# Kernel tuning notes

Measured on AMD Instinct MI355X. Metric: run time of the kernel, lower is better.

Reference implementation:

```python
import jax, jax.numpy as jnp
import numpy as np

D_IN = 2048
D_OUT = 2048
N_HEADS = 32
N_KV = 8
HEAD_DIM = D_OUT // N_HEADS  # 64
CTX = 2048
ROPE_BASE = 10000.0


def _rope_tables(head_dim, ctx, base):
    inv_freq = 1.0 / base ** (np.arange(0, head_dim, 2, dtype=np.float32) / head_dim)
    pos = np.arange(ctx, dtype=np.float32)
    ang = pos[:, None] * inv_freq[None, :]          # [ctx, hd/2]
    ang = np.concatenate([ang, ang], axis=1)         # [ctx, hd]
    return jnp.asarray(np.cos(ang)), jnp.asarray(np.sin(ang))


def _apply_rope(x, cos, sin):
    # x: [b, h, n, hd]; cos/sin: [n, hd]
    half = x.shape[-1] // 2
    x1, x2 = x[..., :half], x[..., half:]
    rotated = jnp.concatenate([-x2, x1], axis=-1)
    return x * cos + rotated * sin


def setup_inputs() -> dict:
    key = jax.random.key(0)
    ks = jax.random.split(key, 5)
    b, n = 1, 2048
    x = jax.random.normal(ks[0], (b, n, D_IN), dtype=jnp.float32)
    s = 0.02
    Wq = jax.random.normal(ks[1], (D_IN, D_OUT), dtype=jnp.float32) * s
    Wk = jax.random.normal(ks[2], (D_IN, N_KV * HEAD_DIM), dtype=jnp.float32) * s
    Wv = jax.random.normal(ks[3], (D_IN, N_KV * HEAD_DIM), dtype=jnp.float32) * s
    Wo = jax.random.normal(ks[4], (D_OUT, D_OUT), dtype=jnp.float32) * s
    cos, sin = _rope_tables(HEAD_DIM, CTX, ROPE_BASE)
    return {"x": x, "Wq": Wq, "Wk": Wk, "Wv": Wv, "Wo": Wo, "cos": cos, "sin": sin}


def reference(x, Wq, Wk, Wv, Wo, cos, sin):
    b, n, _ = x.shape
    gs = N_HEADS // N_KV  # group size
    q = (x @ Wq).reshape(b, n, N_HEADS, HEAD_DIM).transpose(0, 2, 1, 3)  # [b,H,n,d]
    k = (x @ Wk).reshape(b, n, N_KV, HEAD_DIM).transpose(0, 2, 1, 3)     # [b,G,n,d]
    v = (x @ Wv).reshape(b, n, N_KV, HEAD_DIM).transpose(0, 2, 1, 3)
    q = _apply_rope(q, cos[:n], sin[:n])
    k = _apply_rope(k, cos[:n], sin[:n])
    # GQA: view queries as [b, G, gs, n, d]; broadcast K/V over the group axis
    qg = q.reshape(b, N_KV, gs, n, HEAD_DIM)
    scores = jnp.einsum('bgrnd,bgmd->bgrnm', qg, k) / HEAD_DIM ** 0.5
    causal = jnp.triu(jnp.ones((n, n), dtype=bool), k=1)
    scores = jnp.where(causal, -jnp.inf, scores)
    w = jax.nn.softmax(scores, axis=-1)
    ctx = jnp.einsum('bgrnm,bgmd->bgrnd', w, v)           # [b,G,gs,n,d]
    ctx = ctx.reshape(b, N_HEADS, n, HEAD_DIM).transpose(0, 2, 1, 3).reshape(b, n, D_OUT)
    return ctx @ Wo
```

## Files before the change

### kernel.cpp

```cpp
#include <hip/hip_runtime.h>
#include <hip/hip_bf16.h>

typedef __bf16 bf16x8 __attribute__((ext_vector_type(8)));
typedef float f32x4 __attribute__((ext_vector_type(4)));
typedef unsigned u32x4 __attribute__((ext_vector_type(4)));

#define MFMA16 __builtin_amdgcn_mfma_f32_16x16x32_bf16

#define GLD16(gp, lp) __builtin_amdgcn_global_load_lds( \
    (const __attribute__((address_space(1))) void*)(gp), \
    (__attribute__((address_space(3))) void*)(lp), 16, 0, 0)

__device__ __forceinline__ unsigned short f2bf(float f) {
  __hip_bfloat16 h = __float2bfloat16(f);
  return *(unsigned short*)&h;
}
__device__ __forceinline__ float bf2f(unsigned short u) {
  union { unsigned u; float f; } v; v.u = ((unsigned)u) << 16; return v.f;
}

__global__ __launch_bounds__(256)
void convert_bf16_kernel(const float* __restrict__ in, unsigned short* __restrict__ out) {
  int i = blockIdx.x * 256 + threadIdx.x;
  float4 a = *(const float4*)&in[i * 8];
  float4 b = *(const float4*)&in[i * 8 + 4];
  uint4 o;
  o.x = (unsigned)f2bf(a.x) | ((unsigned)f2bf(a.y) << 16);
  o.y = (unsigned)f2bf(a.z) | ((unsigned)f2bf(a.w) << 16);
  o.z = (unsigned)f2bf(b.x) | ((unsigned)f2bf(b.y) << 16);
  o.w = (unsigned)f2bf(b.z) | ((unsigned)f2bf(b.w) << 16);
  *(uint4*)&out[i * 8] = o;
}

__global__ __launch_bounds__(256)
void transpose_bf16_kernel(const float* __restrict__ in, unsigned short* __restrict__ out,
                           int K, int N) {
  __shared__ float tile[64][68];
  const int t = threadIdx.x;
  const int k0 = blockIdx.y * 64, n0 = blockIdx.x * 64;
#pragma unroll
  for (int i = 0; i < 4; ++i) {
    int r = i * 16 + (t >> 4);
    int cc = (t & 15) * 4;
    float4 v = *(const float4*)&in[(k0 + r) * N + n0 + cc];
    tile[r][cc] = v.x; tile[r][cc + 1] = v.y; tile[r][cc + 2] = v.z; tile[r][cc + 3] = v.w;
  }
  __syncthreads();
#pragma unroll
  for (int i = 0; i < 2; ++i) {
    int on = i * 32 + (t >> 3);
    int ok = (t & 7) * 8;
    uint4 o;
    o.x = (unsigned)f2bf(tile[ok + 0][on]) | ((unsigned)f2bf(tile[ok + 1][on]) << 16);
    o.y = (unsigned)f2bf(tile[ok + 2][on]) | ((unsigned)f2bf(tile[ok + 3][on]) << 16);
    o.z = (unsigned)f2bf(tile[ok + 4][on]) | ((unsigned)f2bf(tile[ok + 5][on]) << 16);
    o.w = (unsigned)f2bf(tile[ok + 6][on]) | ((unsigned)f2bf(tile[ok + 7][on]) << 16);
    *(uint4*)&out[(n0 + on) * K + k0 + ok] = o;
  }
}

__global__ __launch_bounds__(256)
void qkv_gemm_kernel(const unsigned short* __restrict__ xb,
                     const unsigned short* __restrict__ Wqt,
                     const unsigned short* __restrict__ Wkt,
                     const unsigned short* __restrict__ Wvt,
                     const float* __restrict__ cosT, const float* __restrict__ sinT,
                     unsigned short* __restrict__ Qb, unsigned short* __restrict__ Kb,
                     unsigned short* __restrict__ Vt)
{
  __shared__ unsigned short Al[2][64 * 64];
  __shared__ unsigned short Bl[2][128 * 64];
  const int t = threadIdx.x;
  const int w = t >> 6, l = t & 63, g = l >> 4, c = l & 15;
  const int wr = w >> 1, wc = w & 1;
  const int r0 = blockIdx.y * 64;
  const int c0 = blockIdx.x * 128;

  const unsigned short* B; int brow0;
  if (c0 < 2048)      { B = Wqt; brow0 = c0; }
  else if (c0 < 2560) { B = Wkt; brow0 = c0 - 2048; }
  else                { B = Wvt; brow0 = c0 - 2560; }

  f32x4 acc[2][4];
#pragma unroll
  for (int m = 0; m < 2; ++m)
#pragma unroll
    for (int n = 0; n < 4; ++n) acc[m][n] = (f32x4){0.f, 0.f, 0.f, 0.f};

  const int srow = t >> 3;
  const int scol = ((t & 7) ^ (srow & 7)) * 8;
  const unsigned dbase = (unsigned)(w * 512);

#define QKV_STAGE(buf, kt_) do {                                              \
    GLD16(&xb[(r0 + srow) * 2048 + (kt_) + scol],        &Al[buf][dbase]);    \
    GLD16(&xb[(r0 + 32 + srow) * 2048 + (kt_) + scol],   &Al[buf][2048 + dbase]); \
    GLD16(&B[(brow0 + srow) * 2048 + (kt_) + scol],      &Bl[buf][dbase]);    \
    GLD16(&B[(brow0 + 32 + srow) * 2048 + (kt_) + scol], &Bl[buf][2048 + dbase]); \
    GLD16(&B[(brow0 + 64 + srow) * 2048 + (kt_) + scol], &Bl[buf][4096 + dbase]); \
    GLD16(&B[(brow0 + 96 + srow) * 2048 + (kt_) + scol], &Bl[buf][6144 + dbase]); \
  } while (0)

  QKV_STAGE(0, 0);
  __syncthreads();

  int cur = 0;
  for (int kt = 0; kt < 2048; kt += 64) {
    if (kt + 64 < 2048) QKV_STAGE(cur ^ 1, kt + 64);
#pragma unroll
    for (int ks = 0; ks < 2; ++ks) {
      const int slot = ((ks * 4 + g) ^ (c & 7)) * 8;
      bf16x8 aF[2], bF[4];
#pragma unroll
      for (int m = 0; m < 2; ++m)
        aF[m] = *(const bf16x8*)&Al[cur][(wr * 32 + m * 16 + c) * 64 + slot];
#pragma unroll
      for (int n = 0; n < 4; ++n)
        bF[n] = *(const bf16x8*)&Bl[cur][(wc * 64 + n * 16 + c) * 64 + slot];
#pragma unroll
      for (int m = 0; m < 2; ++m)
#pragma unroll
        for (int n = 0; n < 4; ++n)
          acc[m][n] = MFMA16(aF[m], bF[n], acc[m][n], 0, 0, 0);
    }
    __syncthreads();
    cur ^= 1;
  }
#undef QKV_STAGE

  const int wcol0 = c0 + wc * 64;
  if (c0 < 2560) {
    unsigned short* dst; int hh;
    if (c0 < 2048) { dst = Qb; hh = wcol0 >> 6; }
    else           { dst = Kb; hh = (wcol0 - 2048) >> 6; }
#pragma unroll
    for (int m = 0; m < 2; ++m) {
#pragma unroll
      for (int j = 0; j < 4; ++j) {
        int p = r0 + wr * 32 + m * 16 + g * 4 + j;
#pragma unroll
        for (int n = 0; n < 2; ++n) {
          int d = n * 16 + c;
          float cv = cosT[p * 64 + d];
          float sv = sinT[p * 64 + d];
          float lo = acc[m][n][j], hi = acc[m][n + 2][j];
          dst[(hh * 2048 + p) * 64 + d]      = f2bf(lo * cv - hi * sv);
          dst[(hh * 2048 + p) * 64 + d + 32] = f2bf(hi * cv + lo * sv);
        }
      }
    }
  } else {
    int kvh = (wcol0 - 2560) >> 6;
#pragma unroll
    for (int m = 0; m < 2; ++m) {
      int p0 = r0 + wr * 32 + m * 16 + g * 4;
      int ps = (p0 & ~0x1C) | ((p0 & 0x0C) << 1) | ((p0 & 0x10) >> 2);
#pragma unroll
      for (int n = 0; n < 4; ++n) {
        int d = n * 16 + c;
        ushort4 u;
        u.x = f2bf(acc[m][n][0]); u.y = f2bf(acc[m][n][1]);
        u.z = f2bf(acc[m][n][2]); u.w = f2bf(acc[m][n][3]);
        *(ushort4*)&Vt[(kvh * 64 + d) * 2048 + ps] = u;
      }
    }
  }
}

__global__ __launch_bounds__(256)
void attn_kernel(const unsigned short* __restrict__ Qb,
                 const unsigned short* __restrict__ Kb,
                 const unsigned short* __restrict__ Vt,
                 unsigned short* __restrict__ ctxB,
                 unsigned short* __restrict__ pExtra,
                 float* __restrict__ ls)
{
  __shared__ unsigned short Kl[2][64 * 64];
  __shared__ unsigned short Vl[2][64 * 64];
  const int t = threadIdx.x, w = t >> 6, l = t & 63, g = l >> 4, c = l & 15;

  static const int slot2cid[32] = {15,16,30,31, 4,13,14,25,26,27,28,29,
                                   11,12,21,22,23,24, 3,9,10,17,18,19,20,
                                   7,8, 2,5,6, 1, 0};
  const int b = blockIdx.x;
  const int h = b & 31;
  const int cid = slot2cid[b >> 5];
  int qt, ci, k;
  if (cid < 5)       { qt = cid;                ci = 0;              k = 1; }
  else if (cid < 17) { qt = 5 + (cid - 5) / 2;  ci = (cid - 5) & 1;  k = 2; }
  else               { qt = 11 + (cid - 17) / 3; ci = (cid - 17) % 3; k = 3; }
  const int NT = 2 * qt + 2;
  const int t0 = (ci * NT) / k;
  const int t1 = ((ci + 1) * NT) / k;

  const int kvh = h >> 2;
  const int qb = qt * 128 + w * 32;
  const int myNT = (qb + 32 + 63) >> 6;

  const float C1 = 0.18033688f;
  const float MB = 23.0831067f;

  const int sr1 = t >> 3;
  const int sr2 = sr1 + 32;
  const int sc1 = ((t & 7) ^ (sr1 & 7)) * 8;
  const int sc2 = ((t & 7) ^ (sr2 & 7)) * 8;
  const unsigned ld1 = (unsigned)t * 8;
  const unsigned ld2 = ld1 + 2048;

  const unsigned short* Kh = Kb + kvh * 2048 * 64;
  const unsigned short* Vh = Vt + kvh * 64 * 2048;

#define ATTN_STAGE(buf, nb_) do {                                  \
    GLD16(&Kh[((nb_) + sr1) * 64 + sc1], &Kl[buf][ld1]);           \
    GLD16(&Kh[((nb_) + sr2) * 64 + sc2], &Kl[buf][ld2]);           \
    GLD16(&Vh[sr1 * 2048 + (nb_) + sc1], &Vl[buf][ld1]);           \
    GLD16(&Vh[sr2 * 2048 + (nb_) + sc2], &Vl[buf][ld2]);           \
  } while (0)

  bf16x8 qf[2][2];
#pragma unroll
  for (int m = 0; m < 2; ++m)
#pragma unroll
    for (int ks = 0; ks < 2; ++ks)
      qf[m][ks] = *(const bf16x8*)&Qb[(h * 2048 + qb + m * 16 + c) * 64 + ks * 32 + g * 8];

  f32x4 ctx[2][4];
  float lsum[2] = {0.f, 0.f};
#pragma unroll
  for (int m = 0; m < 2; ++m)
#pragma unroll
    for (int n = 0; n < 4; ++n) ctx[m][n] = (f32x4){0.f, 0.f, 0.f, 0.f};

  ATTN_STAGE(0, t0 * 64);
  __syncthreads();

  int cur = 0;
  for (int ti = t0; ti < t1; ++ti) {
    if (ti + 1 < t1) ATTN_STAGE(cur ^ 1, (ti + 1) * 64);

    if (ti < myNT) {
      const int kvb = ti * 64;

      f32x4 ST[4][2];
#pragma unroll
      for (int nn = 0; nn < 4; ++nn)
#pragma unroll
        for (int m = 0; m < 2; ++m) ST[nn][m] = (f32x4){0.f, 0.f, 0.f, 0.f};

      __builtin_amdgcn_s_setprio(1);
#pragma unroll
      for (int ks = 0; ks < 2; ++ks) {
        bf16x8 kF[4];
#pragma unroll
        for (int nn = 0; nn < 4; ++nn) {
          int slot = (ks * 4 + g) ^ (c & 7);
          kF[nn] = *(const bf16x8*)&Kl[cur][(nn * 16 + c) * 64 + slot * 8];
        }
#pragma unroll
        for (int nn = 0; nn < 4; ++nn)
#pragma unroll
          for (int m = 0; m < 2; ++m)
            ST[nn][m] = MFMA16(kF[nn], qf[m][ks], ST[nn][m], 0, 0, 0);
      }
      __builtin_amdgcn_s_setprio(0);

      if (kvb + 63 > qb) {
#pragma unroll
        for (int nn = 0; nn < 4; ++nn)
#pragma unroll
          for (int j = 0; j < 4; ++j) {
            int kpos = kvb + nn * 16 + g * 4 + j;
#pragma unroll
            for (int m = 0; m < 2; ++m) {
              int qpos = qb + m * 16 + c;
              if (kpos > qpos) ST[nn][m][j] = -1e30f;
            }
          }
      }

#pragma unroll
      for (int nn = 0; nn < 4; ++nn)
#pragma unroll
        for (int m = 0; m < 2; ++m)
#pragma unroll
          for (int j = 0; j < 4; ++j) {
            float p = exp2f(fmaf(ST[nn][m][j], C1, -MB));
            ST[nn][m][j] = p;
            lsum[m] += p;
          }

      unsigned pk[4][2][2];
#pragma unroll
      for (int nn = 0; nn < 4; ++nn)
#pragma unroll
        for (int m = 0; m < 2; ++m) {
          pk[nn][m][0] = (unsigned)f2bf(ST[nn][m][0]) | ((unsigned)f2bf(ST[nn][m][1]) << 16);
          pk[nn][m][1] = (unsigned)f2bf(ST[nn][m][2]) | ((unsigned)f2bf(ST[nn][m][3]) << 16);
        }

      bf16x8 pa[2][2];
#pragma unroll
      for (int m = 0; m < 2; ++m)
#pragma unroll
        for (int ks = 0; ks < 2; ++ks) {
          u32x4 pw;
          pw[0] = pk[2 * ks][m][0];
          pw[1] = pk[2 * ks][m][1];
          pw[2] = pk[2 * ks + 1][m][0];
          pw[3] = pk[2 * ks + 1][m][1];
          union { u32x4 u; bf16x8 b; } cvt; cvt.u = pw;
          pa[m][ks] = cvt.b;
        }

      __builtin_amdgcn_s_setprio(1);
#pragma unroll
      for (int ks = 0; ks < 2; ++ks) {
        bf16x8 vF[4];
#pragma unroll
        for (int n = 0; n < 4; ++n) {
          int slot = (ks * 4 + g) ^ (c & 7);
          vF[n] = *(const bf16x8*)&Vl[cur][(n * 16 + c) * 64 + slot * 8];
        }
#pragma unroll
        for (int m = 0; m < 2; ++m)
#pragma unroll
          for (int n = 0; n < 4; ++n)
            ctx[m][n] = MFMA16(pa[m][ks], vF[n], ctx[m][n], 0, 0, 0);
      }
      __builtin_amdgcn_s_setprio(0);
    }

    __syncthreads();
    cur ^= 1;
  }
#undef ATTN_STAGE

  unsigned short* pOut; int prstride;
  if (ci == 0) {
    pOut = ctxB + (qt * 128) * 2048 + h * 64;
    prstride = 2048;
  } else {
    int eo = (qt < 11) ? (qt - 5) : (2 * qt - 16);
    pOut = pExtra + (h * 16 + eo + ci - 1) * 8192;
    prstride = 64;
  }
  float* lsOut = ls + (h * 32 + cid) * 128;

#pragma unroll
  for (int m = 0; m < 2; ++m) {
    float rs = lsum[m];
    rs += __shfl_xor(rs, 16);
    rs += __shfl_xor(rs, 32);
    if (l < 16) lsOut[w * 32 + m * 16 + l] = rs;
  }
#pragma unroll
  for (int m = 0; m < 2; ++m)
#pragma unroll
    for (int n = 0; n < 4; ++n)
#pragma unroll
      for (int j = 0; j < 4; ++j) {
        int lr = w * 32 + m * 16 + g * 4 + j;
        int d = n * 16 + c;
        pOut[lr * prstride + d] = f2bf(ctx[m][n][j]);
      }
}

__global__ __launch_bounds__(256)
void combine_kernel(unsigned short* __restrict__ ctxB,
                    const unsigned short* __restrict__ pExtra,
                    const float* __restrict__ ls)
{
  const int idx = (blockIdx.x * 256 + threadIdx.x) * 8;
  const int p = idx >> 11;
  const int col = idx & 2047;
  const int h = col >> 6;
  const int d = col & 63;
  const int qt = p >> 7;
  const int lr = p & 127;

  const int k    = (qt < 5) ? 1 : (qt < 11) ? 2 : 3;
  const int cid0 = (qt < 5) ? qt : (qt < 11) ? (2 * qt - 5) : (3 * qt - 16);
  const int eo   = (qt < 11) ? (qt - 5) : (2 * qt - 16);

  float a[8];
  ushort4 c0 = *(const ushort4*)&ctxB[idx];
  ushort4 c1 = *(const ushort4*)&ctxB[idx + 4];
  a[0] = bf2f(c0.x); a[1] = bf2f(c0.y); a[2] = bf2f(c0.z); a[3] = bf2f(c0.w);
  a[4] = bf2f(c1.x); a[5] = bf2f(c1.y); a[6] = bf2f(c1.z); a[7] = bf2f(c1.w);
  float lt = ls[(h * 32 + cid0) * 128 + lr];

  for (int ci = 1; ci < k; ++ci) {
    lt += ls[(h * 32 + cid0 + ci) * 128 + lr];
    const unsigned short* e = &pExtra[(h * 16 + eo + ci - 1) * 8192 + lr * 64 + d];
    ushort4 e0 = *(const ushort4*)&e[0];
    ushort4 e1 = *(const ushort4*)&e[4];
    a[0] += bf2f(e0.x); a[1] += bf2f(e0.y); a[2] += bf2f(e0.z); a[3] += bf2f(e0.w);
    a[4] += bf2f(e1.x); a[5] += bf2f(e1.y); a[6] += bf2f(e1.z); a[7] += bf2f(e1.w);
  }

  const float inv = 1.f / lt;
  ushort4 o0, o1;
  o0.x = f2bf(a[0] * inv); o0.y = f2bf(a[1] * inv);
  o0.z = f2bf(a[2] * inv); o0.w = f2bf(a[3] * inv);
  o1.x = f2bf(a[4] * inv); o1.y = f2bf(a[5] * inv);
  o1.z = f2bf(a[6] * inv); o1.w = f2bf(a[7] * inv);
  *(ushort4*)&ctxB[idx]     = o0;
  *(ushort4*)&ctxB[idx + 4] = o1;
}

__global__ __launch_bounds__(256)
void out_gemm_kernel(const unsigned short* __restrict__ ctxB,
                     const unsigned short* __restrict__ Wot,
                     float* __restrict__ out)
{
  __shared__ unsigned short Al[2][64 * 64];
  __shared__ unsigned short Bl[2][128 * 64];
  const int t = threadIdx.x;
  const int w = t >> 6, l = t & 63, g = l >> 4, c = l & 15;
  const int wr = w >> 1, wc = w & 1;
  const int r0 = blockIdx.y * 64;
  const int c0 = blockIdx.x * 128;

  f32x4 acc[2][4];
#pragma unroll
  for (int m = 0; m < 2; ++m)
#pragma unroll
    for (int n = 0; n < 4; ++n) acc[m][n] = (f32x4){0.f, 0.f, 0.f, 0.f};

  const int srow = t >> 3;
  const int scol = ((t & 7) ^ (srow & 7)) * 8;
  const unsigned dbase = (unsigned)(w * 512);

#define OUT_STAGE(buf, kt_) do {                                               \
    GLD16(&ctxB[(r0 + srow) * 2048 + (kt_) + scol],      &Al[buf][dbase]);     \
    GLD16(&ctxB[(r0 + 32 + srow) * 2048 + (kt_) + scol], &Al[buf][2048 + dbase]); \
    GLD16(&Wot[(c0 + srow) * 2048 + (kt_) + scol],       &Bl[buf][dbase]);     \
    GLD16(&Wot[(c0 + 32 + srow) * 2048 + (kt_) + scol],  &Bl[buf][2048 + dbase]); \
    GLD16(&Wot[(c0 + 64 + srow) * 2048 + (kt_) + scol],  &Bl[buf][4096 + dbase]); \
    GLD16(&Wot[(c0 + 96 + srow) * 2048 + (kt_) + scol],  &Bl[buf][6144 + dbase]); \
  } while (0)

  OUT_STAGE(0, 0);
  __syncthreads();

  int cur = 0;
  for (int kt = 0; kt < 2048; kt += 64) {
    if (kt + 64 < 2048) OUT_STAGE(cur ^ 1, kt + 64);
#pragma unroll
    for (int ks = 0; ks < 2; ++ks) {
      const int slot = ((ks * 4 + g) ^ (c & 7)) * 8;
      bf16x8 aF[2], bF[4];
#pragma unroll
      for (int m = 0; m < 2; ++m)
        aF[m] = *(const bf16x8*)&Al[cur][(wr * 32 + m * 16 + c) * 64 + slot];
#pragma unroll
      for (int n = 0; n < 4; ++n)
        bF[n] = *(const bf16x8*)&Bl[cur][(wc * 64 + n * 16 + c) * 64 + slot];
#pragma unroll
      for (int m = 0; m < 2; ++m)
#pragma unroll
        for (int n = 0; n < 4; ++n)
          acc[m][n] = MFMA16(aF[m], bF[n], acc[m][n], 0, 0, 0);
    }
    __syncthreads();
    cur ^= 1;
  }
#undef OUT_STAGE

#pragma unroll
  for (int m = 0; m < 2; ++m)
#pragma unroll
    for (int j = 0; j < 4; ++j) {
      int p = r0 + wr * 32 + m * 16 + g * 4 + j;
#pragma unroll
      for (int n = 0; n < 4; ++n)
        out[p * 2048 + c0 + wc * 64 + n * 16 + c] = acc[m][n][j];
    }
}

extern "C" void kernel_launch(void* const* d_in, const int* in_sizes, int n_in,
                              void* d_out, int out_size, void* d_ws, size_t ws_size,
                              hipStream_t stream) {
  const float* x    = (const float*)d_in[0];
  const float* Wq   = (const float*)d_in[1];
  const float* Wk   = (const float*)d_in[2];
  const float* Wv   = (const float*)d_in[3];
  const float* Wo   = (const float*)d_in[4];
  const float* cosT = (const float*)d_in[5];
  const float* sinT = (const float*)d_in[6];
  float* out = (float*)d_out;

  unsigned short* xb     = (unsigned short*)d_ws;
  unsigned short* pExtra = xb;
  unsigned short* Wot    = xb;
  unsigned short* Wqt    = xb + 4 * 1024 * 1024;
  unsigned short* ctxB   = Wqt;
  unsigned short* Wkt    = Wqt + 4 * 1024 * 1024;
  float*          ls     = (float*)Wkt;
  unsigned short* Wvt    = Wkt + 1024 * 1024;
  unsigned short* Qb     = Wvt + 1024 * 1024;
  unsigned short* Kb     = Qb + 4 * 1024 * 1024;
  unsigned short* Vt     = Kb + 1024 * 1024;

  convert_bf16_kernel<<<2048, 256, 0, stream>>>(x, xb);
  transpose_bf16_kernel<<<dim3(32, 32), 256, 0, stream>>>(Wq, Wqt, 2048, 2048);
  transpose_bf16_kernel<<<dim3(8, 32), 256, 0, stream>>>(Wk, Wkt, 2048, 512);
  transpose_bf16_kernel<<<dim3(8, 32), 256, 0, stream>>>(Wv, Wvt, 2048, 512);

  qkv_gemm_kernel<<<dim3(24, 32), 256, 0, stream>>>(xb, Wqt, Wkt, Wvt, cosT, sinT, Qb, Kb, Vt);

  attn_kernel<<<1024, 256, 0, stream>>>(Qb, Kb, Vt, ctxB, pExtra, ls);
  combine_kernel<<<2048, 256, 0, stream>>>(ctxB, pExtra, ls);

  transpose_bf16_kernel<<<dim3(32, 32), 256, 0, stream>>>(Wo, Wot, 2048, 2048);
  out_gemm_kernel<<<dim3(16, 32), 256, 0, stream>>>(ctxB, Wot, out);
}
```

Before: 140.5 us.

## Merge prep and Wo-transpose launches; rebalance attention split-KV work table

Fuses the x conversion and the three weight transposes into a single prep launch. Folds the Wo transpose into the combine kernel, with Wot moved to reuse the Qb buffer. Replaces the attention block-to-work mapping with explicit per-slot tables (qt, t0, t1, ci) that rebalance split ranges and block ordering across CUs. The aim is to cut launch gaps and tail imbalance, at the cost of more intricate, hand-tuned scheduling tables.

```diff
diff --git a/kernel.cpp b/kernel.cpp
--- a/kernel.cpp
+++ b/kernel.cpp
@@ -19,25 +19,10 @@
   union { unsigned u; float f; } v; v.u = ((unsigned)u) << 16; return v.f;
 }
 
-__global__ __launch_bounds__(256)
-void convert_bf16_kernel(const float* __restrict__ in, unsigned short* __restrict__ out) {
-  int i = blockIdx.x * 256 + threadIdx.x;
-  float4 a = *(const float4*)&in[i * 8];
-  float4 b = *(const float4*)&in[i * 8 + 4];
-  uint4 o;
-  o.x = (unsigned)f2bf(a.x) | ((unsigned)f2bf(a.y) << 16);
-  o.y = (unsigned)f2bf(a.z) | ((unsigned)f2bf(a.w) << 16);
-  o.z = (unsigned)f2bf(b.x) | ((unsigned)f2bf(b.y) << 16);
-  o.w = (unsigned)f2bf(b.z) | ((unsigned)f2bf(b.w) << 16);
-  *(uint4*)&out[i * 8] = o;
-}
-
-__global__ __launch_bounds__(256)
-void transpose_bf16_kernel(const float* __restrict__ in, unsigned short* __restrict__ out,
-                           int K, int N) {
+__device__ __forceinline__ void transpose_tile(const float* __restrict__ in,
+                                               unsigned short* __restrict__ out,
+                                               int K, int N, int k0, int n0, int t) {
   __shared__ float tile[64][68];
-  const int t = threadIdx.x;
-  const int k0 = blockIdx.y * 64, n0 = blockIdx.x * 64;
 #pragma unroll
   for (int i = 0; i < 4; ++i) {
     int r = i * 16 + (t >> 4);
@@ -56,6 +41,35 @@
     o.z = (unsigned)f2bf(tile[ok + 4][on]) | ((unsigned)f2bf(tile[ok + 5][on]) << 16);
     o.w = (unsigned)f2bf(tile[ok + 6][on]) | ((unsigned)f2bf(tile[ok + 7][on]) << 16);
     *(uint4*)&out[(n0 + on) * K + k0 + ok] = o;
+  }
+}
+
+__global__ __launch_bounds__(256)
+void prep_kernel(const float* __restrict__ x, const float* __restrict__ Wq,
+                 const float* __restrict__ Wk, const float* __restrict__ Wv,
+                 unsigned short* __restrict__ xb, unsigned short* __restrict__ Wqt,
+                 unsigned short* __restrict__ Wkt, unsigned short* __restrict__ Wvt)
+{
+  const int b = blockIdx.x, t = threadIdx.x;
+  if (b < 2048) {
+    int i = b * 256 + t;
+    float4 a = *(const float4*)&x[i * 8];
+    float4 c = *(const float4*)&x[i * 8 + 4];
+    uint4 o;
+    o.x = (unsigned)f2bf(a.x) | ((unsigned)f2bf(a.y) << 16);
+    o.y = (unsigned)f2bf(a.z) | ((unsigned)f2bf(a.w) << 16);
+    o.z = (unsigned)f2bf(c.x) | ((unsigned)f2bf(c.y) << 16);
+    o.w = (unsigned)f2bf(c.z) | ((unsigned)f2bf(c.w) << 16);
+    *(uint4*)&xb[i * 8] = o;
+  } else if (b < 3072) {
+    int bb = b - 2048;
+    transpose_tile(Wq, Wqt, 2048, 2048, (bb >> 5) * 64, (bb & 31) * 64, t);
+  } else if (b < 3328) {
+    int bb = b - 3072;
+    transpose_tile(Wk, Wkt, 2048, 512, (bb >> 3) * 64, (bb & 7) * 64, t);
+  } else {
+    int bb = b - 3328;
+    transpose_tile(Wv, Wvt, 2048, 512, (bb >> 3) * 64, (bb & 7) * 64, t);
   }
 }
 
@@ -178,19 +192,26 @@
   __shared__ unsigned short Vl[2][64 * 64];
   const int t = threadIdx.x, w = t >> 6, l = t & 63, g = l >> 4, c = l & 15;
 
-  static const int slot2cid[32] = {15,16,30,31, 4,13,14,25,26,27,28,29,
-                                   11,12,21,22,23,24, 3,9,10,17,18,19,20,
-                                   7,8, 2,5,6, 1, 0};
+  static const signed char tab_qt[32] = {
+    10,10, 4, 0,   9, 9,14, 1,  15,15, 2, 5,  15, 8, 8, 5,
+    14,12, 3, 6,  14,12, 7, 6,  13, 7,11,11,  13,13,12,11 };
+  static const signed char tab_t0[32] = {
+     0,11, 0, 0,   0,10, 0, 0,   0,11, 0, 0,  22, 0, 9, 6,
+    10, 0, 0, 0,  20, 9, 0, 7,   0, 8, 0, 8,  10,19,18,16 };
+  static const signed char tab_t1[32] = {
+    11,22,10, 2,  10,20,10, 4,  11,22, 6, 6,  32, 9,18,12,
+    20, 9, 8, 7,  30,18, 8,14,  10,16, 8,16,  19,28,26,24 };
+  static const signed char tab_ci[32] = {
+     0, 1, 0, 0,   0, 1, 0, 0,   0, 1, 0, 0,   2, 0, 1, 1,
+     1, 0, 0, 0,   2, 1, 0, 1,   0, 1, 0, 1,   1, 2, 2, 2 };
+
   const int b = blockIdx.x;
-  const int h = b & 31;
-  const int cid = slot2cid[b >> 5];
-  int qt, ci, k;
-  if (cid < 5)       { qt = cid;                ci = 0;              k = 1; }
-  else if (cid < 17) { qt = 5 + (cid - 5) / 2;  ci = (cid - 5) & 1;  k = 2; }
-  else               { qt = 11 + (cid - 17) / 3; ci = (cid - 17) % 3; k = 3; }
-  const int NT = 2 * qt + 2;
-  const int t0 = (ci * NT) / k;
-  const int t1 = ((ci + 1) * NT) / k;
+  const int h = (b & 255) >> 3;
+  const int idx = (b & 7) * 4 + (b >> 8);
+  const int qt = tab_qt[idx];
+  const int t0 = tab_t0[idx];
+  const int t1 = tab_t1[idx];
+  const int ci = tab_ci[idx];
 
   const int kvh = h >> 2;
   const int qb = qt * 128 + w * 32;
@@ -339,11 +360,11 @@
     pOut = ctxB + (qt * 128) * 2048 + h * 64;
     prstride = 2048;
   } else {
-    int eo = (qt < 11) ? (qt - 5) : (2 * qt - 16);
-    pOut = pExtra + (h * 16 + eo + ci - 1) * 8192;
+    int eo = (qt < 11) ? (qt - 5) : (6 + 2 * (qt - 11) + (ci - 1));
+    pOut = pExtra + (h * 16 + eo) * 8192;
     prstride = 64;
   }
-  float* lsOut = ls + (h * 32 + cid) * 128;
+  float* lsOut = ls + ((h * 16 + qt) * 3 + ci) * 128;
 
 #pragma unroll
   for (int m = 0; m < 2; ++m) {
@@ -365,46 +386,51 @@
 }
 
 __global__ __launch_bounds__(256)
-void combine_kernel(unsigned short* __restrict__ ctxB,
-                    const unsigned short* __restrict__ pExtra,
-                    const float* __restrict__ ls)
+void combine_wo_kernel(unsigned short* __restrict__ ctxB,
+                       const unsigned short* __restrict__ pExtra,
+                       const float* __restrict__ ls,
+                       const float* __restrict__ Wo, unsigned short* __restrict__ Wot)
 {
-  const int idx = (blockIdx.x * 256 + threadIdx.x) * 8;
-  const int p = idx >> 11;
-  const int col = idx & 2047;
-  const int h = col >> 6;
-  const int d = col & 63;
-  const int qt = p >> 7;
-  const int lr = p & 127;
-
-  const int k    = (qt < 5) ? 1 : (qt < 11) ? 2 : 3;
-  const int cid0 = (qt < 5) ? qt : (qt < 11) ? (2 * qt - 5) : (3 * qt - 16);
-  const int eo   = (qt < 11) ? (qt - 5) : (2 * qt - 16);
-
-  float a[8];
-  ushort4 c0 = *(const ushort4*)&ctxB[idx];
-  ushort4 c1 = *(const ushort4*)&ctxB[idx + 4];
-  a[0] = bf2f(c0.x); a[1] = bf2f(c0.y); a[2] = bf2f(c0.z); a[3] = bf2f(c0.w);
-  a[4] = bf2f(c1.x); a[5] = bf2f(c1.y); a[6] = bf2f(c1.z); a[7] = bf2f(c1.w);
-  float lt = ls[(h * 32 + cid0) * 128 + lr];
-
-  for (int ci = 1; ci < k; ++ci) {
-    lt += ls[(h * 32 + cid0 + ci) * 128 + lr];
-    const unsigned short* e = &pExtra[(h * 16 + eo + ci - 1) * 8192 + lr * 64 + d];
-    ushort4 e0 = *(const ushort4*)&e[0];
-    ushort4 e1 = *(const ushort4*)&e[4];
-    a[0] += bf2f(e0.x); a[1] += bf2f(e0.y); a[2] += bf2f(e0.z); a[3] += bf2f(e0.w);
-    a[4] += bf2f(e1.x); a[5] += bf2f(e1.y); a[6] += bf2f(e1.z); a[7] += bf2f(e1.w);
-  }
-
-  const float inv = 1.f / lt;
-  ushort4 o0, o1;
-  o0.x = f2bf(a[0] * inv); o0.y = f2bf(a[1] * inv);
-  o0.z = f2bf(a[2] * inv); o0.w = f2bf(a[3] * inv);
-  o1.x = f2bf(a[4] * inv); o1.y = f2bf(a[5] * inv);
-  o1.z = f2bf(a[6] * inv); o1.w = f2bf(a[7] * inv);
-  *(ushort4*)&ctxB[idx]     = o0;
-  *(ushort4*)&ctxB[idx + 4] = o1;
+  const int b = blockIdx.x, t = threadIdx.x;
+  if (b < 2048) {
+    const int idx = (b * 256 + t) * 8;
+    const int p = idx >> 11;
+    const int col = idx & 2047;
+    const int h = col >> 6;
+    const int d = col & 63;
+    const int qt = p >> 7;
+    const int lr = p & 127;
+    const int k = (qt < 5) ? 1 : (qt < 11) ? 2 : 3;
+
+    float a[8];
+    ushort4 c0 = *(const ushort4*)&ctxB[idx];
+    ushort4 c1 = *(const ushort4*)&ctxB[idx + 4];
+    a[0] = bf2f(c0.x); a[1] = bf2f(c0.y); a[2] = bf2f(c0.z); a[3] = bf2f(c0.w);
+    a[4] = bf2f(c1.x); a[5] = bf2f(c1.y); a[6] = bf2f(c1.z); a[7] = bf2f(c1.w);
+    float lt = ls[((h * 16 + qt) * 3 + 0) * 128 + lr];
+
+    for (int ci = 1; ci < k; ++ci) {
+      lt += ls[((h * 16 + qt) * 3 + ci) * 128 + lr];
+      int eo = (qt < 11) ? (qt - 5) : (6 + 2 * (qt - 11) + (ci - 1));
+      const unsigned short* e = &pExtra[(h * 16 + eo) * 8192 + lr * 64 + d];
+      ushort4 e0 = *(const ushort4*)&e[0];
+      ushort4 e1 = *(const ushort4*)&e[4];
+      a[0] += bf2f(e0.x); a[1] += bf2f(e0.y); a[2] += bf2f(e0.z); a[3] += bf2f(e0.w);
+      a[4] += bf2f(e1.x); a[5] += bf2f(e1.y); a[6] += bf2f(e1.z); a[7] += bf2f(e1.w);
+    }
+
+    const float inv = 1.f / lt;
+    ushort4 o0, o1;
+    o0.x = f2bf(a[0] * inv); o0.y = f2bf(a[1] * inv);
+    o0.z = f2bf(a[2] * inv); o0.w = f2bf(a[3] * inv);
+    o1.x = f2bf(a[4] * inv); o1.y = f2bf(a[5] * inv);
+    o1.z = f2bf(a[6] * inv); o1.w = f2bf(a[7] * inv);
+    *(ushort4*)&ctxB[idx]     = o0;
+    *(ushort4*)&ctxB[idx + 4] = o1;
+  } else {
+    int bb = b - 2048;
+    transpose_tile(Wo, Wot, 2048, 2048, (bb >> 5) * 64, (bb & 31) * 64, t);
+  }
 }
 
 __global__ __launch_bounds__(256)
@@ -491,26 +517,23 @@
 
   unsigned short* xb     = (unsigned short*)d_ws;
   unsigned short* pExtra = xb;
-  unsigned short* Wot    = xb;
   unsigned short* Wqt    = xb + 4 * 1024 * 1024;
   unsigned short* ctxB   = Wqt;
   unsigned short* Wkt    = Wqt + 4 * 1024 * 1024;
   float*          ls     = (float*)Wkt;
   unsigned short* Wvt    = Wkt + 1024 * 1024;
   unsigned short* Qb     = Wvt + 1024 * 1024;
+  unsigned short* Wot    = Qb;
   unsigned short* Kb     = Qb + 4 * 1024 * 1024;
   unsigned short* Vt     = Kb + 1024 * 1024;
 
-  convert_bf16_kernel<<<2048, 256, 0, stream>>>(x, xb);
-  transpose_bf16_kernel<<<dim3(32, 32), 256, 0, stream>>>(Wq, Wqt, 2048, 2048);
-  transpose_bf16_kernel<<<dim3(8, 32), 256, 0, stream>>>(Wk, Wkt, 2048, 512);
-  transpose_bf16_kernel<<<dim3(8, 32), 256, 0, stream>>>(Wv, Wvt, 2048, 512);
+  prep_kernel<<<3584, 256, 0, stream>>>(x, Wq, Wk, Wv, xb, Wqt, Wkt, Wvt);
 
   qkv_gemm_kernel<<<dim3(24, 32), 256, 0, stream>>>(xb, Wqt, Wkt, Wvt, cosT, sinT, Qb, Kb, Vt);
 
   attn_kernel<<<1024, 256, 0, stream>>>(Qb, Kb, Vt, ctxB, pExtra, ls);
-  combine_kernel<<<2048, 256, 0, stream>>>(ctxB, pExtra, ls);
-
-  transpose_bf16_kernel<<<dim3(32, 32), 256, 0, stream>>>(Wo, Wot, 2048, 2048);
+
+  combine_wo_kernel<<<3072, 256, 0, stream>>>(ctxB, pExtra, ls, Wo, Wot);
+
   out_gemm_kernel<<<dim3(16, 32), 256, 0, stream>>>(ctxB, Wot, out);
 }
```

After: 130.5 us. -7.1%, faster.
